# Optimization experiments

Measured on AMD Instinct MI355X. Metric: run time of the kernel, lower is better.

Reference implementation:

```python
import jax, jax.numpy as jnp
import numpy as np

B, N, D = 4, 2048, 1024
H, HD = 16, 64
S = 11  # n_scales
D4 = jnp.array([0.4829629131445341, 0.8365163037378079,
                0.2241438680420134, -0.1294095225512604], dtype=jnp.float32)


def _causal_dilated_d4(f, d):
    """Causal depthwise D4 conv with dilation d along axis 2. f: [B,H,N,HD].
    Matches torch F.pad(x,(3d,0)) + F.conv1d(dilation=d, groups=C):
    y[n] = sum_t D4[t] * f[n - (3-t)*d]."""
    n = f.shape[2]
    fp = jnp.pad(f, ((0, 0), (0, 0), (3 * d, 0), (0, 0)))
    return (D4[0] * fp[:, :, 0:n, :]
            + D4[1] * fp[:, :, d:d + n, :]
            + D4[2] * fp[:, :, 2 * d:2 * d + n, :]
            + D4[3] * fp[:, :, 3 * d:3 * d + n, :])


def setup_inputs() -> dict:
    key = jax.random.key(0)
    ks = jax.random.split(key, 10)
    s = 0.02
    return {
        "x": jax.random.normal(ks[0], (B, N, D), dtype=jnp.float32),
        "Wqkv": jax.random.normal(ks[1], (3 * D, D), dtype=jnp.float32) * s,
        "bqkv": jnp.zeros((3 * D,), dtype=jnp.float32),
        "Wo": jax.random.normal(ks[2], (D, D), dtype=jnp.float32) * s,
        "bo": jnp.zeros((D,), dtype=jnp.float32),
        "Wg": jax.random.normal(ks[3], (D, D), dtype=jnp.float32) * s,
        "bg": jnp.full((D,), 2.0, dtype=jnp.float32),
        "scale_gain": jnp.zeros((S, H), dtype=jnp.float32),
        "Wqs": jax.random.normal(ks[4], (S, HD), dtype=jnp.float32) * 0.01,
        "field_coupling": jnp.eye(H, dtype=jnp.float32)
        + 0.01 * jax.random.normal(ks[5], (H, H), dtype=jnp.float32),
    }


def reference(x, Wqkv, bqkv, Wo, bo, Wg, bg, scale_gain, Wqs, field_coupling):
    b, n, d = x.shape
    qkv = x @ Wqkv.T + bqkv                          # [B,N,3D]
    q, k, v = jnp.split(qkv, 3, axis=-1)
    q = q.reshape(b, n, H, HD).transpose(0, 2, 1, 3)  # [B,H,N,HD]
    k = k.reshape(b, n, H, HD).transpose(0, 2, 1, 3)
    v = v.reshape(b, n, H, HD).transpose(0, 2, 1, 3)

    # per-position scale gains: learned prior + query-conditioned offset
    q_offset = jnp.einsum('bhnd,sd->bhns', q, Wqs)    # [B,H,N,S]
    prior = scale_gain.T[None, :, None, :]            # [1,H,1,S]
    gains = jax.nn.softmax(q_offset + prior, axis=-1)

    # deposit: field[i] = V[i] * ||K[i]||
    k_mag = jnp.linalg.norm(k, axis=-1, keepdims=True)
    field = v * k_mag                                 # [B,H,N,HD]

    # propagate: causal multiscale dilated D4 conv, gain-weighted accumulate
    out_field = jnp.zeros_like(field)
    for j in range(S):
        y = _causal_dilated_d4(field, 1 << j)
        out_field = out_field + gains[:, :, :, j:j + 1] * y

    coupling = jax.nn.softmax(field_coupling, axis=-1)
    out_field = jnp.einsum('ij,bjnd->bind', coupling, out_field)

    gate = jax.nn.sigmoid(x @ Wg.T + bg)              # [B,N,D]
    gathered = out_field.transpose(0, 2, 1, 3).reshape(b, n, d)
    return (gathered * gate) @ Wo.T + bo
```

## Files before the change

kernel.cpp:

```cpp
#include <hip/hip_runtime.h>
#include <hip/hip_bf16.h>
#include <stdint.h>
#include <math.h>

#define BB 4
#define NN 2048
#define DD 1024
#define HH 16
#define HDD 64
#define SS 11

#define D4_0 0.4829629131445341f
#define D4_1 0.8365163037378079f
#define D4_2 0.2241438680420134f
#define D4_3 (-0.1294095225512604f)

typedef __bf16 bf16_t;
typedef __bf16 bf16x4_t __attribute__((ext_vector_type(4)));
typedef __bf16 bf16x8_t __attribute__((ext_vector_type(8)));
typedef float f32x4_t __attribute__((ext_vector_type(4)));

__global__ __launch_bounds__(256) void cvt_all_k(const float* __restrict__ s0,
                                                 const float* __restrict__ s1,
                                                 const float* __restrict__ s2,
                                                 const float* __restrict__ s3,
                                                 bf16_t* __restrict__ d0,
                                                 bf16_t* __restrict__ d1,
                                                 bf16_t* __restrict__ d2,
                                                 bf16_t* __restrict__ d3) {
  const int n0 = 2097152, n1 = 786432, n2 = 262144, n3 = 262144;
  int i = blockIdx.x * 256 + threadIdx.x;
  const float* s;
  bf16_t* d;
  if (i < n0) { s = s0; d = d0; }
  else if (i < n0 + n1) { i -= n0; s = s1; d = d1; }
  else if (i < n0 + n1 + n2) { i -= n0 + n1; s = s2; d = d2; }
  else { i -= n0 + n1 + n2; if (i >= n3) return; s = s3; d = d3; }
  f32x4_t v = ((const f32x4_t*)s)[i];
  bf16x4_t o;
  o[0] = (bf16_t)v[0]; o[1] = (bf16_t)v[1]; o[2] = (bf16_t)v[2]; o[3] = (bf16_t)v[3];
  ((bf16x4_t*)d)[i] = o;
}

__device__ __forceinline__ void gload16(const void* g, void* l) {
  __builtin_amdgcn_global_load_lds((__attribute__((address_space(1))) void*)(void*)g,
                                   (__attribute__((address_space(3))) void*)l,
                                   16, 0, 0);
}

template <int MODE>
__global__ __launch_bounds__(256) void gemm_nt(const bf16_t* __restrict__ A,
                                               const bf16_t* __restrict__ Bw,
                                               const float* __restrict__ bias0,
                                               const float* __restrict__ bias1,
                                               void* __restrict__ out0v,
                                               void* __restrict__ out1v,
                                               int M, int Nn, int K) {
  __shared__ bf16_t As[128 * 64];
  __shared__ bf16_t Bs[128 * 64];

  const int tid = threadIdx.x;
  const int ntiles = Nn >> 7;
  const int grp = ntiles << 3;
  const int g = blockIdx.x / grp;
  const int j = blockIdx.x % grp;
  const int mtile = (g << 3) | (j & 7);
  const int ntile = j >> 3;
  const int row0 = mtile << 7;
  const int col0 = ntile << 7;
  const int w = tid >> 6, lane = tid & 63;
  const int wm = w >> 1, wn = w & 1;
  const int m16 = lane & 15, quad = lane >> 4;

  f32x4_t acc[4][4];
#pragma unroll
  for (int i = 0; i < 4; i++)
#pragma unroll
    for (int jj = 0; jj < 4; jj++) acc[i][jj] = (f32x4_t){0.f, 0.f, 0.f, 0.f};

  for (int kb = 0; kb < K; kb += 64) {
    __syncthreads();
#pragma unroll
    for (int r = 0; r < 4; ++r) {
      int c = r * 256 + tid;
      int row = c >> 3, kc = c & 7;
      int swz = kc ^ (row & 7);
      const bf16_t* gpA = A + (size_t)(row0 + row) * K + kb + swz * 8;
      const bf16_t* gpB = Bw + (size_t)(col0 + row) * K + kb + swz * 8;
      bf16_t* lpA = As + (size_t)(r * 256 + (tid & 192)) * 8;
      bf16_t* lpB = Bs + (size_t)(r * 256 + (tid & 192)) * 8;
      gload16(gpA, lpA);
      gload16(gpB, lpB);
    }
    __syncthreads();

#pragma unroll
    for (int kk = 0; kk < 2; ++kk) {
      bf16x8_t af[4], bfr[4];
      const int kc = (kk << 2) + quad;
#pragma unroll
      for (int i = 0; i < 4; i++) {
        int arow = (wm << 6) + (i << 4) + m16;
        af[i] = *(const bf16x8_t*)(As + arow * 64 + ((kc ^ (arow & 7)) << 3));
        int brow = (wn << 6) + (i << 4) + m16;
        bfr[i] = *(const bf16x8_t*)(Bs + brow * 64 + ((kc ^ (brow & 7)) << 3));
      }
#pragma unroll
      for (int i = 0; i < 4; i++)
#pragma unroll
        for (int jj = 0; jj < 4; jj++)
          acc[i][jj] = __builtin_amdgcn_mfma_f32_16x16x32_bf16(af[i], bfr[jj], acc[i][jj], 0, 0, 0);
    }
  }

#pragma unroll
  for (int i = 0; i < 4; i++) {
#pragma unroll
    for (int jj = 0; jj < 4; jj++) {
      const int grow0 = row0 + (wm << 6) + (i << 4) + (quad << 2);
      const int gcol = col0 + (wn << 6) + (jj << 4) + m16;
      const float bval = (MODE == 0)
                             ? (gcol < 3072 ? bias0[gcol] : bias1[gcol - 3072])
                             : bias0[gcol];
#pragma unroll
      for (int r = 0; r < 4; r++) {
        float val = acc[i][jj][r] + bval;
        if (MODE == 0) {
          if (gcol < 3072)
            ((bf16_t*)out0v)[(size_t)(grow0 + r) * 3072 + gcol] = (bf16_t)val;
          else
            ((bf16_t*)out1v)[(size_t)(grow0 + r) * 1024 + (gcol - 3072)] =
                (bf16_t)(1.f / (1.f + __expf(-val)));
        } else {
          ((float*)out0v)[(size_t)(grow0 + r) * Nn + gcol] = val;
        }
      }
    }
  }
}

__global__ __launch_bounds__(256) void field_gains_k(const bf16_t* __restrict__ qkvb,
                                                     const float* __restrict__ scale_gain,
                                                     const float* __restrict__ Wqs,
                                                     bf16_t* __restrict__ fieldb,
                                                     float* __restrict__ gains) {
  __shared__ float skmag[4 * 16];
  const int tid = threadIdx.x;
  const int w = tid >> 6, lane = tid & 63;
  const int bn = blockIdx.x * 4 + w;
  const int b = bn >> 11, n_pos = bn & 2047;
  const int m16 = lane & 15, quad = lane >> 4;
  const bf16_t* qp = qkvb + (size_t)bn * 3072;

  bf16x8_t aq[2], ak[2], bw[2];
#pragma unroll
  for (int it = 0; it < 2; it++) {
    const int koff = it * 32 + quad * 8;
    aq[it] = *(const bf16x8_t*)(qp + m16 * 64 + koff);
    ak[it] = *(const bf16x8_t*)(qp + 1024 + m16 * 64 + koff);
    bf16x8_t bwv;
    if (m16 < SS) {
      const float* wp = Wqs + m16 * 64 + koff;
#pragma unroll
      for (int j = 0; j < 8; j++) bwv[j] = (bf16_t)wp[j];
    } else {
#pragma unroll
      for (int j = 0; j < 8; j++) bwv[j] = (bf16_t)0.f;
    }
    bw[it] = bwv;
  }

  f32x4_t acc_l = (f32x4_t){0.f, 0.f, 0.f, 0.f};
  f32x4_t acc_k = (f32x4_t){0.f, 0.f, 0.f, 0.f};
#pragma unroll
  for (int it = 0; it < 2; it++) {
    acc_l = __builtin_amdgcn_mfma_f32_16x16x32_bf16(aq[it], bw[it], acc_l, 0, 0, 0);
    acc_k = __builtin_amdgcn_mfma_f32_16x16x32_bf16(ak[it], ak[it], acc_k, 0, 0, 0);
  }

#pragma unroll
  for (int r = 0; r < 4; r++) {
    if (m16 == quad * 4 + r) skmag[w * 16 + m16] = sqrtf(fmaxf(acc_k[r], 0.f));
  }

#pragma unroll
  for (int r = 0; r < 4; r++) {
    const int m = quad * 4 + r;
    float lg = (m16 < SS) ? (acc_l[r] + scale_gain[m16 * 16 + m]) : -1e30f;
    float mx = lg;
#pragma unroll
    for (int sh = 1; sh < 16; sh <<= 1) mx = fmaxf(mx, __shfl_xor(mx, sh, 64));
    float e = (m16 < SS) ? __expf(lg - mx) : 0.f;
    float se = e;
#pragma unroll
    for (int sh = 1; sh < 16; sh <<= 1) se += __shfl_xor(se, sh, 64);
    if (m16 < SS)
      gains[((size_t)(b * 16 + m) * 2048 + n_pos) * SS + m16] = e / se;
  }

  __syncthreads();

#pragma unroll
  for (int h = 0; h < 16; h++) {
    const float km = skmag[w * 16 + h];
    const float v = (float)qp[2048 + h * 64 + lane];
    fieldb[((size_t)(b * 16 + h) * 2048 + n_pos) * 64 + lane] = (bf16_t)(v * km);
  }
}

__global__ __launch_bounds__(256) void conv_k(const bf16_t* __restrict__ field,
                                              const float* __restrict__ gains,
                                              bf16_t* __restrict__ facc) {
  __shared__ float sg[32 * SS];
  const int tid = threadIdx.x;
  const int blk = blockIdx.x;
  const int bh = blk & 63;
  const int ntile = blk >> 6;
  const int n0 = ntile * 32;

  for (int i = tid; i < 32 * SS; i += 256)
    sg[i] = gains[((size_t)bh * 2048 + n0) * SS + i];
  __syncthreads();

  const int w = tid >> 6, lane = tid & 63;
  const int nsub = lane >> 3, c = lane & 7;
  const int ln = w * 8 + nsub;
  const int n = n0 + ln;
  const bf16_t* frow = field + (size_t)bh * 2048 * 64;

  float g[SS];
#pragma unroll
  for (int s = 0; s < SS; s++) g[s] = sg[ln * SS + s];

  float acc[8];
  {
    bf16x8_t f0 = *(const bf16x8_t*)(frow + (size_t)n * 64 + c * 8);
#pragma unroll
    for (int q = 0; q < 8; q++) acc[q] = D4_3 * (float)f0[q];
  }
#pragma unroll
  for (int j = 0; j < 11; j++) {
    float wgt = D4_2 * g[j];
    if (j >= 1) wgt += D4_1 * g[j - 1];
    int rr = n - (1 << j);
    float wv = rr >= 0 ? wgt : 0.f;
    rr = rr >= 0 ? rr : 0;
    bf16x8_t fv = *(const bf16x8_t*)(frow + (size_t)rr * 64 + c * 8);
#pragma unroll
    for (int q = 0; q < 8; q++) acc[q] += wv * (float)fv[q];
  }
#pragma unroll
  for (int j = 0; j < 10; j++) {
    int rr = n - (3 << j);
    float wv = rr >= 0 ? (D4_0 * g[j]) : 0.f;
    rr = rr >= 0 ? rr : 0;
    bf16x8_t fv = *(const bf16x8_t*)(frow + (size_t)rr * 64 + c * 8);
#pragma unroll
    for (int q = 0; q < 8; q++) acc[q] += wv * (float)fv[q];
  }
  bf16x8_t o;
#pragma unroll
  for (int q = 0; q < 8; q++) o[q] = (bf16_t)acc[q];
  *(bf16x8_t*)(facc + ((size_t)bh * 2048 + n) * 64 + c * 8) = o;
}

__global__ __launch_bounds__(1024) void couple_gate_k(const bf16_t* __restrict__ facc,
                                                      const float* __restrict__ fcoup,
                                                      const bf16_t* __restrict__ gate,
                                                      bf16_t* __restrict__ gmat) {
  __shared__ float sacc[1024];
  __shared__ float sc[256];
  __shared__ float scn[256];
  const int tid = threadIdx.x;
  const int bn = blockIdx.x;
  const int b = bn >> 11, n = bn & 2047;
  if (tid < 256) sc[tid] = fcoup[tid];
  const int i = tid >> 6, hd = tid & 63;
  sacc[tid] = (float)facc[(((size_t)(b * 16 + i)) * 2048 + n) * 64 + hd];
  __syncthreads();
  if (tid < 16) {
    float row[16];
    float mx = -1e30f;
#pragma unroll
    for (int j = 0; j < 16; j++) { row[j] = sc[tid * 16 + j]; mx = fmaxf(mx, row[j]); }
    float se = 0.f;
#pragma unroll
    for (int j = 0; j < 16; j++) { row[j] = __expf(row[j] - mx); se += row[j]; }
    float inv = 1.f / se;
#pragma unroll
    for (int j = 0; j < 16; j++) scn[tid * 16 + j] = row[j] * inv;
  }
  __syncthreads();
  float s = 0.f;
#pragma unroll
  for (int j = 0; j < 16; j++) s += scn[i * 16 + j] * sacc[j * 64 + hd];
  const float gt = (float)gate[(size_t)bn * 1024 + tid];
  gmat[(size_t)bn * 1024 + tid] = (bf16_t)(s * gt);
}

extern "C" void kernel_launch(void* const* d_in, const int* in_sizes, int n_in,
                              void* d_out, int out_size, void* d_ws, size_t ws_size,
                              hipStream_t stream) {
  (void)in_sizes; (void)n_in; (void)out_size; (void)ws_size;
  const float* x = (const float*)d_in[0];
  const float* Wqkv = (const float*)d_in[1];
  const float* bqkv = (const float*)d_in[2];
  const float* Wo = (const float*)d_in[3];
  const float* bo = (const float*)d_in[4];
  const float* Wg = (const float*)d_in[5];
  const float* bg = (const float*)d_in[6];
  const float* scale_gain = (const float*)d_in[7];
  const float* Wqs = (const float*)d_in[8];
  const float* fcoup = (const float*)d_in[9];

  char* ws = (char*)d_ws;
  size_t off = 0;
  auto alloc = [&](size_t bytes) {
    void* p = ws + off;
    off += (bytes + 255) & ~(size_t)255;
    return p;
  };
  bf16_t* xb = (bf16_t*)alloc(8192ull * 1024 * 2);
  bf16_t* Wab = (bf16_t*)alloc(4096ull * 1024 * 2);
  bf16_t* Wob = (bf16_t*)alloc(1024ull * 1024 * 2);
  bf16_t* qkvb = (bf16_t*)alloc(8192ull * 3072 * 2);
  bf16_t* gateb = (bf16_t*)alloc(8192ull * 1024 * 2);
  bf16_t* fieldb = (bf16_t*)alloc(8388608ull * 2);
  float* gains = (float*)alloc(8192ull * 16 * SS * 4);
  bf16_t* facc = (bf16_t*)alloc(8388608ull * 2);
  bf16_t* gmat = (bf16_t*)alloc(8192ull * 1024 * 2);

  cvt_all_k<<<13316, 256, 0, stream>>>(x, Wqkv, Wg, Wo,
                                       xb, Wab, Wab + 3072ull * 1024, Wob);

  gemm_nt<0><<<64 * 32, 256, 0, stream>>>(xb, Wab, bqkv, bg, qkvb, gateb, 8192, 4096, 1024);

  field_gains_k<<<2048, 256, 0, stream>>>(qkvb, scale_gain, Wqs, fieldb, gains);

  conv_k<<<4096, 256, 0, stream>>>(fieldb, gains, facc);

  couple_gate_k<<<8192, 1024, 0, stream>>>(facc, fcoup, gateb, gmat);

  gemm_nt<1><<<64 * 8, 256, 0, stream>>>(gmat, Wob, bo, nullptr, (void*)d_out, nullptr, 8192, 1024, 1024);
}
```

Baseline: 287.7 us.

## Replace QKV+gate GEMM with 256x256-tile, 8-wave pipelined MFMA kernel

Adds a dedicated 256x256-tile GEMM with 512 threads, double-buffered LDS, half-tile async global-to-LDS staging interleaved with MFMA phases, and s_setprio scheduling for the fused QKV+gate projection. The larger tile raises arithmetic intensity and cuts redundant global loads compared with the 128x128 generic kernel. It also remaps block order by XCD for L2 locality. The risk is lower occupancy from high LDS and register use, and hand-written waitcnt choreography that could be fragile.

```diff
diff --git a/kernel.cpp b/kernel.cpp
--- a/kernel.cpp
+++ b/kernel.cpp
@@ -48,6 +48,162 @@
                                    16, 0, 0);
 }
 
+__global__ __launch_bounds__(512, 2) void gemm256(const bf16_t* __restrict__ Aa,
+                                                  const bf16_t* __restrict__ Bw,
+                                                  const float* __restrict__ bias0,
+                                                  const float* __restrict__ bias1,
+                                                  bf16_t* __restrict__ out0,
+                                                  bf16_t* __restrict__ out1) {
+  __shared__ bf16_t sA[2][16384];
+  __shared__ bf16_t sB[2][16384];
+
+  const int tid = threadIdx.x;
+  const int s = (blockIdx.x & 7) * 64 + (blockIdx.x >> 3);
+  const int mtile = s >> 4;
+  const int ntile = s & 15;
+  const int row0 = mtile << 8;
+  const int col0 = ntile << 8;
+
+  const int w = tid >> 6, lane = tid & 63;
+  const int wm = w >> 2, wn = w & 3;
+  const int wmbase = wm << 7;
+  const int wnbase = wn << 6;
+  const int m16 = lane & 15, quad = lane >> 4;
+
+  f32x4_t acc[8][4];
+#pragma unroll
+  for (int i = 0; i < 8; i++)
+#pragma unroll
+    for (int jq = 0; jq < 4; jq++) acc[i][jq] = (f32x4_t){0.f, 0.f, 0.f, 0.f};
+
+  auto stage_half = [&](int buf, int tensor, int half, int t) {
+    if (t >= 16) return;
+    const bf16_t* gb = tensor ? Bw : Aa;
+    const int gr0 = (tensor ? col0 : row0) + (half << 7);
+    const int kb = t << 6;
+    bf16_t* lbase = (tensor ? sB[buf] : sA[buf]) + (half << 13);
+#pragma unroll
+    for (int l = 0; l < 2; ++l) {
+      int c = l * 512 + tid;
+      int row = c >> 3, kc = c & 7;
+      int swz = kc ^ (row & 7);
+      const bf16_t* g = gb + (size_t)(gr0 + row) * 1024 + kb + swz * 8;
+      bf16_t* lp = lbase + ((l * 512 + (tid & 448)) << 3);
+      gload16(g, lp);
+    }
+  };
+
+  bf16x8_t af[4], bfr[4];
+  auto rdA = [&](int buf, int ih, int ks) {
+#pragma unroll
+    for (int i = 0; i < 4; i++) {
+      int ar = wmbase + ((ih * 4 + i) << 4) + m16;
+      int kc = (ks << 2) + quad;
+      af[i] = *(const bf16x8_t*)&sA[buf][ar * 64 + ((kc ^ (ar & 7)) << 3)];
+    }
+  };
+  auto rdB = [&](int buf, int ks) {
+#pragma unroll
+    for (int jq = 0; jq < 4; jq++) {
+      int br = wnbase + (jq << 4) + m16;
+      int kc = (ks << 2) + quad;
+      bfr[jq] = *(const bf16x8_t*)&sB[buf][br * 64 + ((kc ^ (br & 7)) << 3)];
+    }
+  };
+  auto domfma = [&](int ih) {
+#pragma unroll
+    for (int i = 0; i < 4; i++)
+#pragma unroll
+      for (int jq = 0; jq < 4; jq++)
+        acc[ih * 4 + i][jq] =
+            __builtin_amdgcn_mfma_f32_16x16x32_bf16(af[i], bfr[jq], acc[ih * 4 + i][jq], 0, 0, 0);
+  };
+
+#define PH_ENTER()                                        \
+  __builtin_amdgcn_sched_barrier(0);                      \
+  __builtin_amdgcn_s_barrier();                           \
+  asm volatile("s_waitcnt lgkmcnt(0)" ::: "memory");      \
+  __builtin_amdgcn_sched_barrier(0);                      \
+  __builtin_amdgcn_s_setprio(1)
+#define PH_EXIT()                                         \
+  __builtin_amdgcn_s_setprio(0);                          \
+  __builtin_amdgcn_sched_barrier(0);                      \
+  __builtin_amdgcn_s_barrier()
+#define PH_EXIT_V2()                                      \
+  __builtin_amdgcn_s_setprio(0);                          \
+  __builtin_amdgcn_sched_barrier(0);                      \
+  asm volatile("s_waitcnt vmcnt(2)" ::: "memory");        \
+  __builtin_amdgcn_sched_barrier(0);                      \
+  __builtin_amdgcn_s_barrier()
+#define PH_EXIT_V0()                                      \
+  __builtin_amdgcn_s_setprio(0);                          \
+  __builtin_amdgcn_sched_barrier(0);                      \
+  asm volatile("s_waitcnt vmcnt(0)" ::: "memory");        \
+  __builtin_amdgcn_sched_barrier(0);                      \
+  __builtin_amdgcn_s_barrier()
+
+  stage_half(0, 0, 0, 0); stage_half(0, 0, 1, 0);
+  stage_half(0, 1, 0, 0); stage_half(0, 1, 1, 0);
+  stage_half(1, 1, 0, 1);
+  asm volatile("s_waitcnt vmcnt(2)" ::: "memory");
+  __builtin_amdgcn_sched_barrier(0);
+  __builtin_amdgcn_s_barrier();
+
+  for (int it = 0; it < 8; ++it) {
+    const int O = 2 * it + 1, E2 = 2 * it + 2, O2 = 2 * it + 3;
+    rdA(0, 0, 0); rdB(0, 0);
+    stage_half(1, 1, 1, O);
+    PH_ENTER(); domfma(0); PH_EXIT();
+    rdA(0, 1, 0);
+    stage_half(1, 0, 0, O);
+    PH_ENTER(); domfma(1); PH_EXIT();
+    rdA(0, 0, 1); rdB(0, 1);
+    stage_half(1, 0, 1, O);
+    PH_ENTER(); domfma(0); PH_EXIT();
+    rdA(0, 1, 1);
+    stage_half(0, 1, 0, E2);
+    PH_ENTER(); domfma(1);
+    if (E2 < 16) { PH_EXIT_V2(); } else { PH_EXIT_V0(); }
+    rdA(1, 0, 0); rdB(1, 0);
+    stage_half(0, 1, 1, E2);
+    PH_ENTER(); domfma(0); PH_EXIT();
+    rdA(1, 1, 0);
+    stage_half(0, 0, 0, E2);
+    PH_ENTER(); domfma(1); PH_EXIT();
+    rdA(1, 0, 1); rdB(1, 1);
+    stage_half(0, 0, 1, E2);
+    PH_ENTER(); domfma(0); PH_EXIT();
+    rdA(1, 1, 1);
+    stage_half(1, 1, 0, O2);
+    PH_ENTER(); domfma(1);
+    if (O2 < 16) { PH_EXIT_V2(); } else { PH_EXIT_V0(); }
+  }
+#undef PH_ENTER
+#undef PH_EXIT
+#undef PH_EXIT_V2
+#undef PH_EXIT_V0
+
+  const bool is_gate = (col0 >= 3072);
+#pragma unroll
+  for (int i = 0; i < 8; i++) {
+#pragma unroll
+    for (int jq = 0; jq < 4; jq++) {
+      const int grow0 = row0 + wmbase + (i << 4) + (quad << 2);
+      const int gcol = col0 + wnbase + (jq << 4) + m16;
+      const float bval = is_gate ? bias1[gcol - 3072] : bias0[gcol];
+#pragma unroll
+      for (int r = 0; r < 4; r++) {
+        float val = acc[i][jq][r] + bval;
+        if (is_gate)
+          out1[(size_t)(grow0 + r) * 1024 + (gcol - 3072)] =
+              (bf16_t)(1.f / (1.f + __expf(-val)));
+        else
+          out0[(size_t)(grow0 + r) * 3072 + gcol] = (bf16_t)val;
+      }
+    }
+  }
+}
+
 template <int MODE>
 __global__ __launch_bounds__(256) void gemm_nt(const bf16_t* __restrict__ A,
                                                const bf16_t* __restrict__ Bw,
@@ -333,7 +489,7 @@
   cvt_all_k<<<13316, 256, 0, stream>>>(x, Wqkv, Wg, Wo,
                                        xb, Wab, Wab + 3072ull * 1024, Wob);
 
-  gemm_nt<0><<<64 * 32, 256, 0, stream>>>(xb, Wab, bqkv, bg, qkvb, gateb, 8192, 4096, 1024);
+  gemm256<<<512, 512, 0, stream>>>(xb, Wab, bqkv, bg, qkvb, gateb);
 
   field_gains_k<<<2048, 256, 0, stream>>>(qkvb, scale_gain, Wqs, fieldb, gains);
 
```

Measured after the change: 277.9 us. 1.04x faster.
